# Kernel optimization log

Measured on AMD Instinct MI355X. Metric: run time of the kernel, lower is better.

## Reference

```python
import jax, jax.numpy as jnp
import numpy as np

H = 512      # hidden_size
Z = 128      # z_dim
E = 512      # embedding_dim
D = 2 * H + Z  # GRU hidden / decoder state dim = 1152
V = 32000    # output_size
BS = 256
N = 128      # encoder nodes per source


def setup_inputs() -> dict:
    key = jax.random.key(0)
    ks = jax.random.split(key, 24)
    s = 0.05
    inp = {
        "prev_y": jax.random.normal(ks[0], (BS, E), jnp.float32),
        "prev_h": jax.random.normal(ks[1], (BS, D), jnp.float32),
        "equ_enc": jax.random.normal(ks[2], (BS, N, H), jnp.float32),
        "sns_enc": jax.random.normal(ks[3], (BS, N, H), jnp.float32),
        "z_sample": jax.random.normal(ks[4], (BS, Z), jnp.float32),
        "equ_mask": jax.random.randint(ks[5], (BS, N), 0, 2) > 0,
        "sns_mask": jax.random.randint(ks[6], (BS, N), 0, 2) > 0,
        # Attention (equ): W1: HxH, W2: HxD, vt: 1xH (torch Linear weight = [out,in])
        "W1e": jax.random.normal(ks[7], (H, H), jnp.float32) * s,
        "W2e": jax.random.normal(ks[8], (H, D), jnp.float32) * s,
        "vte": jax.random.normal(ks[9], (1, H), jnp.float32) * s,
        "W1s": jax.random.normal(ks[10], (H, H), jnp.float32) * s,
        "W2s": jax.random.normal(ks[11], (H, D), jnp.float32) * s,
        "vts": jax.random.normal(ks[12], (1, H), jnp.float32) * s,
        "plan_W": jax.random.normal(ks[13], (2, D), jnp.float32) * s,
        "plan_b": jax.random.normal(ks[14], (2,), jnp.float32) * s,
        "Wc": jax.random.normal(ks[15], (H, E + H), jnp.float32) * s,
        "bc": jax.random.normal(ks[16], (H,), jnp.float32) * s,
        # GRU: input H -> hidden D
        "w_ih": jax.random.normal(ks[17], (3 * D, H), jnp.float32) * s,
        "w_hh": jax.random.normal(ks[18], (3 * D, D), jnp.float32) * s,
        "b_ih": jax.random.normal(ks[19], (3 * D,), jnp.float32) * s,
        "b_hh": jax.random.normal(ks[20], (3 * D,), jnp.float32) * s,
        "Wout": jax.random.normal(ks[21], (V, D), jnp.float32) * s,
        "bout": jax.random.normal(ks[22], (V,), jnp.float32) * s,
    }
    return inp


def _attn(h, enc, mask, W1, W2, vt):
    # enc: (b,n,H), h: (b,D)
    et = jnp.einsum('bnh,kh->bnk', enc, W1)          # (b,n,H)
    dt = (h @ W2.T)[:, None, :]                       # (b,1,H)
    u = jnp.einsum('bnh,h->bn', jnp.tanh(et + dt), vt[0])
    u = jnp.where(mask, -jnp.inf, u)
    return jax.nn.softmax(u, axis=-1)                 # (b,n)


def reference(prev_y, prev_h, equ_enc, sns_enc, z_sample, equ_mask, sns_mask,
              W1e, W2e, vte, W1s, W2s, vts, plan_W, plan_b, Wc, bc,
              w_ih, w_hh, b_ih, b_hh, Wout, bout):
    aw_e = _attn(prev_h, equ_enc, equ_mask, W1e, W2e, vte)
    ctx_e = jnp.einsum('bn,bnh->bh', aw_e, equ_enc)
    aw_s = _attn(prev_h, sns_enc, sns_mask, W1s, W2s, vts)
    ctx_s = jnp.einsum('bn,bnh->bh', aw_s, sns_enc)
    plan = jax.nn.softmax(prev_h @ plan_W.T + plan_b, axis=-1)  # (b,2)
    combine = jnp.stack([ctx_e, ctx_s], axis=1)                  # (b,2,H)
    context = jnp.einsum('bk,bkh->bh', plan, combine)
    y_ctx = jnp.concatenate([prev_y, context], axis=-1)          # (b,E+H)
    x = y_ctx @ Wc.T + bc                                        # (b,H)
    # single-step GRU (torch gate order: r, z, n)
    gx = x @ w_ih.T + b_ih                                       # (b,3D)
    gh = prev_h @ w_hh.T + b_hh
    Dh = prev_h.shape[-1]
    gx_r, gx_z, gx_n = gx[:, :Dh], gx[:, Dh:2*Dh], gx[:, 2*Dh:]
    gh_r, gh_z, gh_n = gh[:, :Dh], gh[:, Dh:2*Dh], gh[:, 2*Dh:]
    r = jax.nn.sigmoid(gx_r + gh_r)
    zg = jax.nn.sigmoid(gx_z + gh_z)
    n = jnp.tanh(gx_n + r * gh_n)
    h_new = (1.0 - zg) * n + zg * prev_h                          # (b,D)
    dec_output = (h_new @ Wout.T + bout)[:, None, :]              # (b,1,V)
    dec_hidden = h_new[None]                                      # (1,b,D)
    return dec_output, dec_hidden, plan
```

## Files before the change

kernel.cpp:

```cpp
#include <hip/hip_runtime.h>
#include <stdint.h>
#include <math.h>

#define BS_  256
#define NSEQ 128
#define HH   512
#define DD   1152
#define VV   32000
#define BN_  (BS_*NSEQ)

typedef float  f32x4  __attribute__((ext_vector_type(4)));
typedef __bf16 bf16x8 __attribute__((ext_vector_type(8)));

__device__ __forceinline__ f32x4 mfma16(bf16x8 a, bf16x8 b, f32x4 c) {
    return __builtin_amdgcn_mfma_f32_16x16x32_bf16(a, b, c, 0, 0, 0);
}

__device__ __forceinline__ bf16x8 pack8(f32x4 a, f32x4 b) {
    bf16x8 v;
    v[0] = (__bf16)a[0]; v[1] = (__bf16)a[1]; v[2] = (__bf16)a[2]; v[3] = (__bf16)a[3];
    v[4] = (__bf16)b[0]; v[5] = (__bf16)b[1]; v[6] = (__bf16)b[2]; v[7] = (__bf16)b[3];
    return v;
}

__global__ __launch_bounds__(256) void k_gemm_bias(
    const float* __restrict__ A, const float* __restrict__ B,
    const float* __restrict__ bias, float* __restrict__ C,
    int K, int ldc)
{
    const int cb = blockIdx.x * 64;
    const int rb = blockIdx.y * 64;
    const int t  = threadIdx.x;
    const int w = t >> 6, lane = t & 63, g = lane >> 4, r = lane & 15;
    const int s_row = t >> 2, s_kc = t & 3;

    __shared__ bf16x8 sm[2][2][256];

    const float* Ap = A + (size_t)(rb + s_row) * K + s_kc * 8;
    const float* Bp = B + (size_t)(cb + s_row) * K + s_kc * 8;

    const int KS = K >> 5;
    f32x4 pa0 = *(const f32x4*)Ap, pa1 = *(const f32x4*)(Ap + 4);
    f32x4 pb0 = *(const f32x4*)Bp, pb1 = *(const f32x4*)(Bp + 4);

    f32x4 acc[4] = {{0,0,0,0},{0,0,0,0},{0,0,0,0},{0,0,0,0}};

    for (int kb = 0; kb < KS; ++kb) {
        sm[kb & 1][0][s_kc * 64 + s_row] = pack8(pa0, pa1);
        sm[kb & 1][1][s_kc * 64 + s_row] = pack8(pb0, pb1);
        __syncthreads();
        if (kb + 1 < KS) {
            const float* a2 = Ap + (kb + 1) * 32;
            const float* b2 = Bp + (kb + 1) * 32;
            pa0 = *(const f32x4*)a2; pa1 = *(const f32x4*)(a2 + 4);
            pb0 = *(const f32x4*)b2; pb1 = *(const f32x4*)(b2 + 4);
        }
        bf16x8 af = sm[kb & 1][0][g * 64 + w * 16 + r];
        #pragma unroll
        for (int j = 0; j < 4; ++j) {
            bf16x8 bf = sm[kb & 1][1][g * 64 + j * 16 + r];
            acc[j] = mfma16(af, bf, acc[j]);
        }
    }
    #pragma unroll
    for (int j = 0; j < 4; ++j) {
        int col = cb + j * 16 + r;
        float bv = bias ? bias[col] : 0.f;
        #pragma unroll
        for (int q = 0; q < 4; ++q) {
            int row = rb + w * 16 + g * 4 + q;
            C[(size_t)row * ldc + col] = acc[j][q] + bv;
        }
    }
}

__global__ __launch_bounds__(256) void k_prevh(
    const float* __restrict__ prev_h, const float* __restrict__ W2e,
    const float* __restrict__ W2s, const float* __restrict__ w_hh,
    const float* __restrict__ b_hh,
    float* __restrict__ dt_e, float* __restrict__ dt_s, float* __restrict__ gh)
{
    const int cb = blockIdx.x * 64;
    const int rb = blockIdx.y * 64;
    const int t  = threadIdx.x;
    const int w = t >> 6, lane = t & 63, g = lane >> 4, r = lane & 15;
    const int s_row = t >> 2, s_kc = t & 3;
    const int K = DD;

    __shared__ bf16x8 sm[2][2][256];

    const float* Ap = prev_h + (size_t)(rb + s_row) * K + s_kc * 8;
    const float* Bp;
    {
        int brow = cb + s_row;
        if (cb < 512)        Bp = W2e + (size_t)brow * K;
        else if (cb < 1024)  Bp = W2s + (size_t)(brow - 512) * K;
        else                 Bp = w_hh + (size_t)(brow - 1024) * K;
        Bp += s_kc * 8;
    }

    const int KS = K >> 5;
    f32x4 pa0 = *(const f32x4*)Ap, pa1 = *(const f32x4*)(Ap + 4);
    f32x4 pb0 = *(const f32x4*)Bp, pb1 = *(const f32x4*)(Bp + 4);

    f32x4 acc[4] = {{0,0,0,0},{0,0,0,0},{0,0,0,0},{0,0,0,0}};

    for (int kb = 0; kb < KS; ++kb) {
        sm[kb & 1][0][s_kc * 64 + s_row] = pack8(pa0, pa1);
        sm[kb & 1][1][s_kc * 64 + s_row] = pack8(pb0, pb1);
        __syncthreads();
        if (kb + 1 < KS) {
            const float* a2 = Ap + (kb + 1) * 32;
            const float* b2 = Bp + (kb + 1) * 32;
            pa0 = *(const f32x4*)a2; pa1 = *(const f32x4*)(a2 + 4);
            pb0 = *(const f32x4*)b2; pb1 = *(const f32x4*)(b2 + 4);
        }
        bf16x8 af = sm[kb & 1][0][g * 64 + w * 16 + r];
        #pragma unroll
        for (int j = 0; j < 4; ++j) {
            bf16x8 bf = sm[kb & 1][1][g * 64 + j * 16 + r];
            acc[j] = mfma16(af, bf, acc[j]);
        }
    }

    #pragma unroll
    for (int j = 0; j < 4; ++j) {
        int col = cb + j * 16 + r;
        #pragma unroll
        for (int q = 0; q < 4; ++q) {
            int row = rb + w * 16 + g * 4 + q;
            float v = acc[j][q];
            if (cb < 512)       dt_e[(size_t)row * 512 + col] = v;
            else if (cb < 1024) dt_s[(size_t)row * 512 + (col - 512)] = v;
            else {
                int c0 = col - 1024;
                gh[(size_t)row * 3456 + c0] = v + b_hh[c0];
            }
        }
    }
}

__global__ __launch_bounds__(512) void k_attn_u(
    const float* __restrict__ enc_e, const float* __restrict__ enc_s,
    const float* __restrict__ W1e, const float* __restrict__ W1s,
    const float* __restrict__ vte, const float* __restrict__ vts,
    const float* __restrict__ dt_e, const float* __restrict__ dt_s,
    float* __restrict__ u)
{
    extern __shared__ char smem_raw[];
    bf16x8* As  = (bf16x8*)smem_raw;
    bf16x8* Bs  = (bf16x8*)(smem_raw + 65536);
    float*  dts = (float*)(smem_raw + 131072);
    float*  vtl = dts + 512;
    float*  uacc = vtl + 512;

    const int e = blockIdx.y;
    const float* enc = e ? enc_s : enc_e;
    const float* W1  = e ? W1s : W1e;
    const float* vt  = e ? vts : vte;
    const float* dt  = e ? dt_s : dt_e;

    const int rowbase = blockIdx.x * 64;
    const int b = rowbase >> 7;
    const int t = threadIdx.x;
    const int w = t >> 6, lane = t & 63, g = lane >> 4, r = lane & 15;

    if (t < 64) uacc[t] = 0.f;
    dts[t] = dt[(size_t)b * 512 + t];
    vtl[t] = vt[t];

    #pragma unroll
    for (int i = 0; i < 8; ++i) {
        int row = w * 8 + i;
        const float* src = enc + (size_t)(rowbase + row) * 512 + lane * 8;
        f32x4 x0 = *(const f32x4*)src;
        f32x4 x1 = *(const f32x4*)(src + 4);
        As[lane * 64 + (row ^ (lane & 15))] = pack8(x0, x1);
    }

    f32x4 p0[4], p1[4];
    {
        int cc = 0, kb = 0;
        #pragma unroll
        for (int jj = 0; jj < 4; ++jj) {
            int c = t + 512 * jj;
            int col = c >> 3, kc = c & 7;
            const float* src = W1 + (size_t)(cc * 256 + col) * 512 + kb * 64 + kc * 8;
            p0[jj] = *(const f32x4*)src;
            p1[jj] = *(const f32x4*)(src + 4);
        }
    }

    f32x4 acc[4][2];
    #pragma unroll
    for (int i = 0; i < 4; ++i) { acc[i][0] = (f32x4){0,0,0,0}; acc[i][1] = (f32x4){0,0,0,0}; }

    for (int s = 0; s < 16; ++s) {
        bf16x8* Bb = Bs + (s & 1) * 2048;
        #pragma unroll
        for (int jj = 0; jj < 4; ++jj) {
            int c = t + 512 * jj;
            int col = c >> 3, kc = c & 7;
            Bb[kc * 256 + col] = pack8(p0[jj], p1[jj]);
        }
        __syncthreads();
        if (s + 1 < 16) {
            int cc2 = (s + 1) >> 3, kb2 = (s + 1) & 7;
            #pragma unroll
            for (int jj = 0; jj < 4; ++jj) {
                int c = t + 512 * jj;
                int col = c >> 3, kc = c & 7;
                const float* src = W1 + (size_t)(cc2 * 256 + col) * 512 + kb2 * 64 + kc * 8;
                p0[jj] = *(const f32x4*)src;
                p1[jj] = *(const f32x4*)(src + 4);
            }
        }
        int kb = s & 7;
        #pragma unroll
        for (int kk = 0; kk < 2; ++kk) {
            int kg = kb * 8 + kk * 4 + g;
            bf16x8 bf0 = Bb[(kk * 4 + g) * 256 + w * 32 + r];
            bf16x8 bf1 = Bb[(kk * 4 + g) * 256 + w * 32 + 16 + r];
            #pragma unroll
            for (int i = 0; i < 4; ++i) {
                bf16x8 af = As[kg * 64 + (16 * i + (r ^ (kg & 15)))];
                acc[i][0] = mfma16(af, bf0, acc[i][0]);
                acc[i][1] = mfma16(af, bf1, acc[i][1]);
            }
        }
        if ((s & 7) == 7) {
            int cc = s >> 3;
            #pragma unroll
            for (int i = 0; i < 4; ++i) {
                float ps0 = 0.f, ps1 = 0.f, ps2 = 0.f, ps3 = 0.f;
                #pragma unroll
                for (int j = 0; j < 2; ++j) {
                    int col = cc * 256 + w * 32 + j * 16 + r;
                    float dv = dts[col], vv = vtl[col];
                    ps0 += vv * tanhf(acc[i][j][0] + dv);
                    ps1 += vv * tanhf(acc[i][j][1] + dv);
                    ps2 += vv * tanhf(acc[i][j][2] + dv);
                    ps3 += vv * tanhf(acc[i][j][3] + dv);
                }
                #pragma unroll
                for (int m = 1; m < 16; m <<= 1) {
                    ps0 += __shfl_xor(ps0, m);
                    ps1 += __shfl_xor(ps1, m);
                    ps2 += __shfl_xor(ps2, m);
                    ps3 += __shfl_xor(ps3, m);
                }
                if (r == 0) {
                    atomicAdd(&uacc[16 * i + 4 * g + 0], ps0);
                    atomicAdd(&uacc[16 * i + 4 * g + 1], ps1);
                    atomicAdd(&uacc[16 * i + 4 * g + 2], ps2);
                    atomicAdd(&uacc[16 * i + 4 * g + 3], ps3);
                }
                acc[i][0] = (f32x4){0,0,0,0};
                acc[i][1] = (f32x4){0,0,0,0};
            }
        }
    }
    __syncthreads();
    if (t < 64) u[(size_t)e * BN_ + rowbase + t] = uacc[t];
}

__global__ __launch_bounds__(256) void k_ctx(
    const float* __restrict__ u, const int* __restrict__ mask_e,
    const int* __restrict__ mask_s, const float* __restrict__ enc_e,
    const float* __restrict__ enc_s, const float* __restrict__ prev_h,
    const float* __restrict__ plan_W, const float* __restrict__ plan_b,
    const float* __restrict__ prev_y,
    float* __restrict__ y_ctx, float* __restrict__ plan_out)
{
    const int b = blockIdx.x;
    const int t = threadIdx.x;
    const int lane = t & 63, wid = t >> 6, half = t >> 7, n = t & 127;

    __shared__ float aw[2][128];
    __shared__ float red[16];
    __shared__ float planv[2];

    const int* mask = half ? mask_s : mask_e;
    float uv = u[(size_t)half * BN_ + b * 128 + n];
    bool msk = mask[b * 128 + n] != 0;
    float val = msk ? -3.4e38f : uv;

    float mx = val;
    #pragma unroll
    for (int m = 1; m < 64; m <<= 1) mx = fmaxf(mx, __shfl_xor(mx, m));
    if (lane == 0) red[wid] = mx;
    __syncthreads();
    mx = fmaxf(red[half * 2], red[half * 2 + 1]);
    float ex = msk ? 0.f : __expf(uv - mx);
    float sm = ex;
    #pragma unroll
    for (int m = 1; m < 64; m <<= 1) sm += __shfl_xor(sm, m);
    if (lane == 0) red[4 + wid] = sm;
    __syncthreads();
    sm = red[4 + half * 2] + red[4 + half * 2 + 1];
    aw[half][n] = ex / sm;

    float p0 = 0.f, p1 = 0.f;
    for (int i = t; i < DD; i += 256) {
        float hv = prev_h[(size_t)b * DD + i];
        p0 += hv * plan_W[i];
        p1 += hv * plan_W[DD + i];
    }
    #pragma unroll
    for (int m = 1; m < 64; m <<= 1) { p0 += __shfl_xor(p0, m); p1 += __shfl_xor(p1, m); }
    if (lane == 0) { red[8 + wid] = p0; red[12 + wid] = p1; }
    __syncthreads();
    if (t == 0) {
        float l0 = red[8] + red[9] + red[10] + red[11] + plan_b[0];
        float l1 = red[12] + red[13] + red[14] + red[15] + plan_b[1];
        float mm = fmaxf(l0, l1);
        float e0 = __expf(l0 - mm), e1 = __expf(l1 - mm);
        float ss = e0 + e1;
        planv[0] = e0 / ss; planv[1] = e1 / ss;
        plan_out[b * 2 + 0] = planv[0];
        plan_out[b * 2 + 1] = planv[1];
    }
    __syncthreads();

    float pl0 = planv[0], pl1 = planv[1];
    #pragma unroll
    for (int cc = 0; cc < 2; ++cc) {
        int col = t + cc * 256;
        float ae = 0.f, as2 = 0.f;
        const float* pe = enc_e + (size_t)b * 128 * 512 + col;
        const float* ps = enc_s + (size_t)b * 128 * 512 + col;
        #pragma unroll 4
        for (int nn = 0; nn < 128; ++nn) {
            ae  += aw[0][nn] * pe[(size_t)nn * 512];
            as2 += aw[1][nn] * ps[(size_t)nn * 512];
        }
        float ctx = pl0 * ae + pl1 * as2;
        y_ctx[(size_t)b * 1024 + col] = prev_y[(size_t)b * 512 + col];
        y_ctx[(size_t)b * 1024 + 512 + col] = ctx;
    }
}

__global__ __launch_bounds__(384) void k_gru(
    const float* __restrict__ gx, const float* __restrict__ gh,
    const float* __restrict__ prev_h, float* __restrict__ h_new,
    float* __restrict__ out_hidden)
{
    int d = blockIdx.x * 384 + threadIdx.x;
    int b = blockIdx.y;
    size_t o3 = (size_t)b * 3456;
    float xr = gx[o3 + d], xz = gx[o3 + 1152 + d], xn = gx[o3 + 2304 + d];
    float hr = gh[o3 + d], hz = gh[o3 + 1152 + d], hn = gh[o3 + 2304 + d];
    float rr = 1.f / (1.f + __expf(-(xr + hr)));
    float zz = 1.f / (1.f + __expf(-(xz + hz)));
    float nv = tanhf(xn + rr * hn);
    float hv = (1.f - zz) * nv + zz * prev_h[(size_t)b * DD + d];
    h_new[(size_t)b * DD + d] = hv;
    out_hidden[(size_t)b * DD + d] = hv;
}

extern "C" void kernel_launch(void* const* d_in, const int* in_sizes, int n_in,
                              void* d_out, int out_size, void* d_ws, size_t ws_size,
                              hipStream_t stream)
{
    const float* prev_y = (const float*)d_in[0];
    const float* prev_h = (const float*)d_in[1];
    const float* enc_e  = (const float*)d_in[2];
    const float* enc_s  = (const float*)d_in[3];
    const int*   mask_e = (const int*)d_in[5];
    const int*   mask_s = (const int*)d_in[6];
    const float* W1e    = (const float*)d_in[7];
    const float* W2e    = (const float*)d_in[8];
    const float* vte    = (const float*)d_in[9];
    const float* W1s    = (const float*)d_in[10];
    const float* W2s    = (const float*)d_in[11];
    const float* vts    = (const float*)d_in[12];
    const float* plan_W = (const float*)d_in[13];
    const float* plan_b = (const float*)d_in[14];
    const float* Wc     = (const float*)d_in[15];
    const float* bc     = (const float*)d_in[16];
    const float* w_ih   = (const float*)d_in[17];
    const float* w_hh   = (const float*)d_in[18];
    const float* b_ih   = (const float*)d_in[19];
    const float* b_hh   = (const float*)d_in[20];
    const float* Wout   = (const float*)d_in[21];
    const float* bout   = (const float*)d_in[22];

    float* out = (float*)d_out;
    float* ws  = (float*)d_ws;
    float* dt_e  = ws;
    float* dt_s  = dt_e + 131072;
    float* gh    = dt_s + 131072;
    float* uu    = gh + 884736;
    float* y_ctx = uu + 65536;
    float* xx    = y_ctx + 262144;
    float* gx    = xx + 131072;
    float* h_new = gx + 884736;

    float* dec_out  = out;
    float* dec_hid  = out + 8192000;
    float* plan_out = out + 8486912;

    k_prevh<<<dim3(70, 4), 256, 0, stream>>>(prev_h, W2e, W2s, w_hh, b_hh,
                                             dt_e, dt_s, gh);

    (void)hipFuncSetAttribute((const void*)k_attn_u,
                              hipFuncAttributeMaxDynamicSharedMemorySize, 143360);
    k_attn_u<<<dim3(BN_ / 64, 2), 512, 135424, stream>>>(
        enc_e, enc_s, W1e, W1s, vte, vts, dt_e, dt_s, uu);

    k_ctx<<<dim3(BS_), 256, 0, stream>>>(uu, mask_e, mask_s, enc_e, enc_s,
                                         prev_h, plan_W, plan_b, prev_y,
                                         y_ctx, plan_out);

    k_gemm_bias<<<dim3(8, 4), 256, 0, stream>>>(y_ctx, Wc, bc, xx, 1024, 512);
    k_gemm_bias<<<dim3(54, 4), 256, 0, stream>>>(xx, w_ih, b_ih, gx, 512, 3456);

    k_gru<<<dim3(3, BS_), 384, 0, stream>>>(gx, gh, prev_h, h_new, dec_hid);

    k_gemm_bias<<<dim3(500, 4), 256, 0, stream>>>(h_new, Wout, bout, dec_out,
                                                  1152, 32000);
}
```

Baseline: 641.8 us.

## Use 128x128 MFMA tiles for large GEMMs and restructure attention and context kernels

Measured after the change: 575.0 us. -10.4%, faster.

```diff
diff --git a/kernel.cpp b/kernel.cpp
--- a/kernel.cpp
+++ b/kernel.cpp
@@ -23,21 +23,117 @@
     return v;
 }
 
-__global__ __launch_bounds__(256) void k_gemm_bias(
+__device__ __forceinline__ float tanh_fast(float x) {
+    float e = __expf(2.f * x);
+    return 1.f - __fdividef(2.f, e + 1.f);
+}
+
+__global__ __launch_bounds__(256) void k_tile128(
     const float* __restrict__ A, const float* __restrict__ B,
     const float* __restrict__ bias, float* __restrict__ C,
     int K, int ldc)
+{
+    const int rb = blockIdx.x * 128;
+    const int cb = blockIdx.y * 128;
+    const int t = threadIdx.x;
+    const int w = t >> 6, wr = w >> 1, wc = w & 1;
+    const int lane = t & 63, g = lane >> 4, r = lane & 15;
+    const int s_row = t >> 1, s_h = t & 1;
+
+    __shared__ bf16x8 sm[2][2][512];
+
+    const float* Ap = A + (size_t)(rb + s_row) * K + s_h * 16;
+    const float* Bp = B + (size_t)(cb + s_row) * K + s_h * 16;
+
+    const int kg0 = 2 * s_h, kg1 = 2 * s_h + 1;
+    const int swz0 = kg0 * 128 + ((s_row & 112) | ((s_row ^ (kg0 << 2)) & 15));
+    const int swz1 = kg1 * 128 + ((s_row & 112) | ((s_row ^ (kg1 << 2)) & 15));
+
+    int ai[4], bi[4];
+    #pragma unroll
+    for (int i = 0; i < 4; ++i) {
+        ai[i] = g * 128 + wr * 64 + i * 16 + ((r ^ (g << 2)) & 15);
+        bi[i] = g * 128 + wc * 64 + i * 16 + ((r ^ (g << 2)) & 15);
+    }
+
+    const int KS = K >> 5;
+    f32x4 pa0 = ((const f32x4*)Ap)[0], pa1 = ((const f32x4*)Ap)[1],
+          pa2 = ((const f32x4*)Ap)[2], pa3 = ((const f32x4*)Ap)[3];
+    f32x4 pb0 = ((const f32x4*)Bp)[0], pb1 = ((const f32x4*)Bp)[1],
+          pb2 = ((const f32x4*)Bp)[2], pb3 = ((const f32x4*)Bp)[3];
+
+    f32x4 acc[4][4];
+    #pragma unroll
+    for (int i = 0; i < 4; ++i)
+        #pragma unroll
+        for (int j = 0; j < 4; ++j) acc[i][j] = (f32x4){0.f, 0.f, 0.f, 0.f};
+
+    for (int kb = 0; kb < KS; ++kb) {
+        const int buf = kb & 1;
+        sm[buf][0][swz0] = pack8(pa0, pa1);
+        sm[buf][0][swz1] = pack8(pa2, pa3);
+        sm[buf][1][swz0] = pack8(pb0, pb1);
+        sm[buf][1][swz1] = pack8(pb2, pb3);
+        __syncthreads();
+        if (kb + 1 < KS) {
+            const float* a2 = Ap + (kb + 1) * 32;
+            const float* b2 = Bp + (kb + 1) * 32;
+            pa0 = ((const f32x4*)a2)[0]; pa1 = ((const f32x4*)a2)[1];
+            pa2 = ((const f32x4*)a2)[2]; pa3 = ((const f32x4*)a2)[3];
+            pb0 = ((const f32x4*)b2)[0]; pb1 = ((const f32x4*)b2)[1];
+            pb2 = ((const f32x4*)b2)[2]; pb3 = ((const f32x4*)b2)[3];
+        }
+        bf16x8 af[4], bfr[4];
+        #pragma unroll
+        for (int i = 0; i < 4; ++i) af[i]  = sm[buf][0][ai[i]];
+        #pragma unroll
+        for (int j = 0; j < 4; ++j) bfr[j] = sm[buf][1][bi[j]];
+        #pragma unroll
+        for (int i = 0; i < 4; ++i)
+            #pragma unroll
+            for (int j = 0; j < 4; ++j)
+                acc[i][j] = mfma16(af[i], bfr[j], acc[i][j]);
+    }
+
+    #pragma unroll
+    for (int j = 0; j < 4; ++j) {
+        const int col = cb + wc * 64 + j * 16 + r;
+        const float bv = bias ? bias[col] : 0.f;
+        #pragma unroll
+        for (int i = 0; i < 4; ++i) {
+            #pragma unroll
+            for (int q = 0; q < 4; ++q) {
+                const int row = rb + wr * 64 + i * 16 + g * 4 + q;
+                C[(size_t)row * ldc + col] = acc[i][j][q] + bv;
+            }
+        }
+    }
+}
+
+__global__ __launch_bounds__(256) void k_prevh(
+    const float* __restrict__ prev_h, const float* __restrict__ W2e,
+    const float* __restrict__ W2s, const float* __restrict__ w_hh,
+    const float* __restrict__ b_hh,
+    float* __restrict__ dt_e, float* __restrict__ dt_s, float* __restrict__ gh)
 {
     const int cb = blockIdx.x * 64;
     const int rb = blockIdx.y * 64;
     const int t  = threadIdx.x;
     const int w = t >> 6, lane = t & 63, g = lane >> 4, r = lane & 15;
     const int s_row = t >> 2, s_kc = t & 3;
+    const int K = DD;
 
     __shared__ bf16x8 sm[2][2][256];
 
-    const float* Ap = A + (size_t)(rb + s_row) * K + s_kc * 8;
-    const float* Bp = B + (size_t)(cb + s_row) * K + s_kc * 8;
+    const float* Ap = prev_h + (size_t)(rb + s_row) * K + s_kc * 8;
+    const float* Bp;
+    {
+        int brow = cb + s_row;
+        if (cb < 512)        Bp = W2e + (size_t)brow * K;
+        else if (cb < 1024)  Bp = W2s + (size_t)(brow - 512) * K;
+        else                 Bp = w_hh + (size_t)(brow - 1024) * K;
+        Bp += s_kc * 8;
+    }
 
     const int KS = K >> 5;
     f32x4 pa0 = *(const f32x4*)Ap, pa1 = *(const f32x4*)(Ap + 4);
@@ -62,66 +158,6 @@
             acc[j] = mfma16(af, bf, acc[j]);
         }
     }
-    #pragma unroll
-    for (int j = 0; j < 4; ++j) {
-        int col = cb + j * 16 + r;
-        float bv = bias ? bias[col] : 0.f;
-        #pragma unroll
-        for (int q = 0; q < 4; ++q) {
-            int row = rb + w * 16 + g * 4 + q;
-            C[(size_t)row * ldc + col] = acc[j][q] + bv;
-        }
-    }
-}
-
-__global__ __launch_bounds__(256) void k_prevh(
-    const float* __restrict__ prev_h, const float* __restrict__ W2e,
-    const float* __restrict__ W2s, const float* __restrict__ w_hh,
-    const float* __restrict__ b_hh,
-    float* __restrict__ dt_e, float* __restrict__ dt_s, float* __restrict__ gh)
-{
-    const int cb = blockIdx.x * 64;
-    const int rb = blockIdx.y * 64;
-    const int t  = threadIdx.x;
-    const int w = t >> 6, lane = t & 63, g = lane >> 4, r = lane & 15;
-    const int s_row = t >> 2, s_kc = t & 3;
-    const int K = DD;
-
-    __shared__ bf16x8 sm[2][2][256];
-
-    const float* Ap = prev_h + (size_t)(rb + s_row) * K + s_kc * 8;
-    const float* Bp;
-    {
-        int brow = cb + s_row;
-        if (cb < 512)        Bp = W2e + (size_t)brow * K;
-        else if (cb < 1024)  Bp = W2s + (size_t)(brow - 512) * K;
-        else                 Bp = w_hh + (size_t)(brow - 1024) * K;
-        Bp += s_kc * 8;
-    }
-
-    const int KS = K >> 5;
-    f32x4 pa0 = *(const f32x4*)Ap, pa1 = *(const f32x4*)(Ap + 4);
-    f32x4 pb0 = *(const f32x4*)Bp, pb1 = *(const f32x4*)(Bp + 4);
-
-    f32x4 acc[4] = {{0,0,0,0},{0,0,0,0},{0,0,0,0},{0,0,0,0}};
-
-    for (int kb = 0; kb < KS; ++kb) {
-        sm[kb & 1][0][s_kc * 64 + s_row] = pack8(pa0, pa1);
-        sm[kb & 1][1][s_kc * 64 + s_row] = pack8(pb0, pb1);
-        __syncthreads();
-        if (kb + 1 < KS) {
-            const float* a2 = Ap + (kb + 1) * 32;
-            const float* b2 = Bp + (kb + 1) * 32;
-            pa0 = *(const f32x4*)a2; pa1 = *(const f32x4*)(a2 + 4);
-            pb0 = *(const f32x4*)b2; pb1 = *(const f32x4*)(b2 + 4);
-        }
-        bf16x8 af = sm[kb & 1][0][g * 64 + w * 16 + r];
-        #pragma unroll
-        for (int j = 0; j < 4; ++j) {
-            bf16x8 bf = sm[kb & 1][1][g * 64 + j * 16 + r];
-            acc[j] = mfma16(af, bf, acc[j]);
-        }
-    }
 
     #pragma unroll
     for (int j = 0; j < 4; ++j) {
@@ -140,128 +176,114 @@
     }
 }
 
-__global__ __launch_bounds__(512) void k_attn_u(
+__global__ __launch_bounds__(256) void k_attn(
     const float* __restrict__ enc_e, const float* __restrict__ enc_s,
     const float* __restrict__ W1e, const float* __restrict__ W1s,
     const float* __restrict__ vte, const float* __restrict__ vts,
     const float* __restrict__ dt_e, const float* __restrict__ dt_s,
     float* __restrict__ u)
 {
-    extern __shared__ char smem_raw[];
-    bf16x8* As  = (bf16x8*)smem_raw;
-    bf16x8* Bs  = (bf16x8*)(smem_raw + 65536);
-    float*  dts = (float*)(smem_raw + 131072);
-    float*  vtl = dts + 512;
-    float*  uacc = vtl + 512;
-
+    const int b = blockIdx.x;
     const int e = blockIdx.y;
     const float* enc = e ? enc_s : enc_e;
-    const float* W1  = e ? W1s : W1e;
-    const float* vt  = e ? vts : vte;
+    const float* W1  = e ? W1s  : W1e;
+    const float* vt  = e ? vts  : vte;
     const float* dt  = e ? dt_s : dt_e;
 
-    const int rowbase = blockIdx.x * 64;
-    const int b = rowbase >> 7;
+    __shared__ bf16x8 sm[2][2][512];
+    __shared__ float uacc[128];
+
     const int t = threadIdx.x;
-    const int w = t >> 6, lane = t & 63, g = lane >> 4, r = lane & 15;
-
-    if (t < 64) uacc[t] = 0.f;
-    dts[t] = dt[(size_t)b * 512 + t];
-    vtl[t] = vt[t];
-
-    #pragma unroll
-    for (int i = 0; i < 8; ++i) {
-        int row = w * 8 + i;
-        const float* src = enc + (size_t)(rowbase + row) * 512 + lane * 8;
-        f32x4 x0 = *(const f32x4*)src;
-        f32x4 x1 = *(const f32x4*)(src + 4);
-        As[lane * 64 + (row ^ (lane & 15))] = pack8(x0, x1);
-    }
-
-    f32x4 p0[4], p1[4];
+    const int w = t >> 6, wr = w >> 1, wc = w & 1;
+    const int lane = t & 63, g = lane >> 4, r = lane & 15;
+    const int s_row = t >> 1, s_h = t & 1;
+
+    if (t < 128) uacc[t] = 0.f;
+
+    const int kg0 = 2 * s_h, kg1 = 2 * s_h + 1;
+    const int swz0 = kg0 * 128 + ((s_row & 112) | ((s_row ^ (kg0 << 2)) & 15));
+    const int swz1 = kg1 * 128 + ((s_row & 112) | ((s_row ^ (kg1 << 2)) & 15));
+
+    int ai[4], bi[4];
+    #pragma unroll
+    for (int i = 0; i < 4; ++i) {
+        ai[i] = g * 128 + wr * 64 + i * 16 + ((r ^ (g << 2)) & 15);
+        bi[i] = g * 128 + wc * 64 + i * 16 + ((r ^ (g << 2)) & 15);
+    }
+
+    const float* Abase = enc + (size_t)(b * 128 + s_row) * 512 + s_h * 16;
+
+    f32x4 pa0, pa1, pa2, pa3, pb0, pb1, pb2, pb3;
     {
-        int cc = 0, kb = 0;
-        #pragma unroll
-        for (int jj = 0; jj < 4; ++jj) {
-            int c = t + 512 * jj;
-            int col = c >> 3, kc = c & 7;
-            const float* src = W1 + (size_t)(cc * 256 + col) * 512 + kb * 64 + kc * 8;
-            p0[jj] = *(const f32x4*)src;
-            p1[jj] = *(const f32x4*)(src + 4);
-        }
-    }
-
-    f32x4 acc[4][2];
-    #pragma unroll
-    for (int i = 0; i < 4; ++i) { acc[i][0] = (f32x4){0,0,0,0}; acc[i][1] = (f32x4){0,0,0,0}; }
-
-    for (int s = 0; s < 16; ++s) {
-        bf16x8* Bb = Bs + (s & 1) * 2048;
-        #pragma unroll
-        for (int jj = 0; jj < 4; ++jj) {
-            int c = t + 512 * jj;
-            int col = c >> 3, kc = c & 7;
-            Bb[kc * 256 + col] = pack8(p0[jj], p1[jj]);
-        }
-        __syncthreads();
-        if (s + 1 < 16) {
-            int cc2 = (s + 1) >> 3, kb2 = (s + 1) & 7;
-            #pragma unroll
-            for (int jj = 0; jj < 4; ++jj) {
-                int c = t + 512 * jj;
-                int col = c >> 3, kc = c & 7;
-                const float* src = W1 + (size_t)(cc2 * 256 + col) * 512 + kb2 * 64 + kc * 8;
-                p0[jj] = *(const f32x4*)src;
-                p1[jj] = *(const f32x4*)(src + 4);
+        const float* ap = Abase;
+        const float* bp = W1 + (size_t)s_row * 512 + s_h * 16;
+        pa0 = ((const f32x4*)ap)[0]; pa1 = ((const f32x4*)ap)[1];
+        pa2 = ((const f32x4*)ap)[2]; pa3 = ((const f32x4*)ap)[3];
+        pb0 = ((const f32x4*)bp)[0]; pb1 = ((const f32x4*)bp)[1];
+        pb2 = ((const f32x4*)bp)[2]; pb3 = ((const f32x4*)bp)[3];
+    }
+
+    for (int nc = 0; nc < 4; ++nc) {
+        f32x4 acc[4][4];
+        #pragma unroll
+        for (int i = 0; i < 4; ++i)
+            #pragma unroll
+            for (int j = 0; j < 4; ++j) acc[i][j] = (f32x4){0.f, 0.f, 0.f, 0.f};
+
+        for (int kb = 0; kb < 16; ++kb) {
+            const int buf = kb & 1;
+            sm[buf][0][swz0] = pack8(pa0, pa1);
+            sm[buf][0][swz1] = pack8(pa2, pa3);
+            sm[buf][1][swz0] = pack8(pb0, pb1);
+            sm[buf][1][swz1] = pack8(pb2, pb3);
+            __syncthreads();
+
+            int nnc = nc, nkb = kb + 1;
+            if (nkb == 16) { nnc = nc + 1; nkb = 0; }
+            if (nnc < 4) {
+                const float* ap = Abase + nkb * 32;
+                const float* bp = W1 + (size_t)(nnc * 128 + s_row) * 512 + nkb * 32 + s_h * 16;
+                pa0 = ((const f32x4*)ap)[0]; pa1 = ((const f32x4*)ap)[1];
+                pa2 = ((const f32x4*)ap)[2]; pa3 = ((const f32x4*)ap)[3];
+                pb0 = ((const f32x4*)bp)[0]; pb1 = ((const f32x4*)bp)[1];
+                pb2 = ((const f32x4*)bp)[2]; pb3 = ((const f32x4*)bp)[3];
             }
-        }
-        int kb = s & 7;
-        #pragma unroll
-        for (int kk = 0; kk < 2; ++kk) {
-            int kg = kb * 8 + kk * 4 + g;
-            bf16x8 bf0 = Bb[(kk * 4 + g) * 256 + w * 32 + r];
-            bf16x8 bf1 = Bb[(kk * 4 + g) * 256 + w * 32 + 16 + r];
-            #pragma unroll
-            for (int i = 0; i < 4; ++i) {
-                bf16x8 af = As[kg * 64 + (16 * i + (r ^ (kg & 15)))];
-                acc[i][0] = mfma16(af, bf0, acc[i][0]);
-                acc[i][1] = mfma16(af, bf1, acc[i][1]);
+
+            bf16x8 af[4], bfr[4];
+            #pragma unroll
+            for (int i = 0; i < 4; ++i) af[i]  = sm[buf][0][ai[i]];
+            #pragma unroll
+            for (int j = 0; j < 4; ++j) bfr[j] = sm[buf][1][bi[j]];
+            #pragma unroll
+            for (int i = 0; i < 4; ++i)
+                #pragma unroll
+                for (int j = 0; j < 4; ++j)
+                    acc[i][j] = mfma16(af[i], bfr[j], acc[i][j]);
+        }
+
+        float dv[4], vv[4];
+        #pragma unroll
+        for (int j = 0; j < 4; ++j) {
+            int col = nc * 128 + wc * 64 + j * 16 + r;
+            dv[j] = dt[(size_t)b * 512 + col];
+            vv[j] = vt[col];
+        }
+        #pragma unroll
+        for (int i = 0; i < 4; ++i) {
+            #pragma unroll
+            for (int q = 0; q < 4; ++q) {
+                float s = 0.f;
+                #pragma unroll
+                for (int j = 0; j < 4; ++j)
+                    s += vv[j] * tanh_fast(acc[i][j][q] + dv[j]);
+                #pragma unroll
+                for (int m = 1; m < 16; m <<= 1) s += __shfl_xor(s, m);
+                if (r == 0) atomicAdd(&uacc[wr * 64 + i * 16 + g * 4 + q], s);
             }
         }
-        if ((s & 7) == 7) {
-            int cc = s >> 3;
-            #pragma unroll
-            for (int i = 0; i < 4; ++i) {
-                float ps0 = 0.f, ps1 = 0.f, ps2 = 0.f, ps3 = 0.f;
-                #pragma unroll
-                for (int j = 0; j < 2; ++j) {
-                    int col = cc * 256 + w * 32 + j * 16 + r;
-                    float dv = dts[col], vv = vtl[col];
-                    ps0 += vv * tanhf(acc[i][j][0] + dv);
-                    ps1 += vv * tanhf(acc[i][j][1] + dv);
-                    ps2 += vv * tanhf(acc[i][j][2] + dv);
-                    ps3 += vv * tanhf(acc[i][j][3] + dv);
-                }
-                #pragma unroll
-                for (int m = 1; m < 16; m <<= 1) {
-                    ps0 += __shfl_xor(ps0, m);
-                    ps1 += __shfl_xor(ps1, m);
-                    ps2 += __shfl_xor(ps2, m);
-                    ps3 += __shfl_xor(ps3, m);
-                }
-                if (r == 0) {
-                    atomicAdd(&uacc[16 * i + 4 * g + 0], ps0);
-                    atomicAdd(&uacc[16 * i + 4 * g + 1], ps1);
-                    atomicAdd(&uacc[16 * i + 4 * g + 2], ps2);
-                    atomicAdd(&uacc[16 * i + 4 * g + 3], ps3);
-                }
-                acc[i][0] = (f32x4){0,0,0,0};
-                acc[i][1] = (f32x4){0,0,0,0};
-            }
-        }
     }
     __syncthreads();
-    if (t < 64) u[(size_t)e * BN_ + rowbase + t] = uacc[t];
+    if (t < 128) u[(size_t)e * BN_ + b * 128 + t] = uacc[t];
 }
 
 __global__ __launch_bounds__(256) void k_ctx(
@@ -323,20 +345,68 @@
     __syncthreads();
 
     float pl0 = planv[0], pl1 = planv[1];
-    #pragma unroll
-    for (int cc = 0; cc < 2; ++cc) {
-        int col = t + cc * 256;
-        float ae = 0.f, as2 = 0.f;
-        const float* pe = enc_e + (size_t)b * 128 * 512 + col;
-        const float* ps = enc_s + (size_t)b * 128 * 512 + col;
-        #pragma unroll 4
-        for (int nn = 0; nn < 128; ++nn) {
-            ae  += aw[0][nn] * pe[(size_t)nn * 512];
-            as2 += aw[1][nn] * ps[(size_t)nn * 512];
-        }
-        float ctx = pl0 * ae + pl1 * as2;
-        y_ctx[(size_t)b * 1024 + col] = prev_y[(size_t)b * 512 + col];
-        y_ctx[(size_t)b * 1024 + 512 + col] = ctx;
+    int col = blockIdx.y * 256 + t;
+    float ae = 0.f, as2 = 0.f;
+    const float* pe = enc_e + (size_t)b * 128 * 512 + col;
+    const float* ps = enc_s + (size_t)b * 128 * 512 + col;
+    #pragma unroll 8
+    for (int nn = 0; nn < 128; ++nn) {
+        ae  += aw[0][nn] * pe[(size_t)nn * 512];
+        as2 += aw[1][nn] * ps[(size_t)nn * 512];
+    }
+    float ctx = pl0 * ae + pl1 * as2;
+    y_ctx[(size_t)b * 1024 + col] = prev_y[(size_t)b * 512 + col];
+    y_ctx[(size_t)b * 1024 + 512 + col] = ctx;
+}
+
+__global__ __launch_bounds__(256) void k_gemm_bias(
+    const float* __restrict__ A, const float* __restrict__ B,
+    const float* __restrict__ bias, float* __restrict__ C,
+    int K, int ldc)
+{
+    const int cb = blockIdx.x * 64;
+    const int rb = blockIdx.y * 64;
+    const int t  = threadIdx.x;
+    const int w = t >> 6, lane = t & 63, g = lane >> 4, r = lane & 15;
+    const int s_row = t >> 2, s_kc = t & 3;
+
+    __shared__ bf16x8 sm[2][2][256];
+
+    const float* Ap = A + (size_t)(rb + s_row) * K + s_kc * 8;
+    const float* Bp = B + (size_t)(cb + s_row) * K + s_kc * 8;
+
+    const int KS = K >> 5;
+    f32x4 pa0 = *(const f32x4*)Ap, pa1 = *(const f32x4*)(Ap + 4);
+    f32x4 pb0 = *(const f32x4*)Bp, pb1 = *(const f32x4*)(Bp + 4);
+
+    f32x4 acc[4] = {{0,0,0,0},{0,0,0,0},{0,0,0,0},{0,0,0,0}};
+
+    for (int kb = 0; kb < KS; ++kb) {
+        sm[kb & 1][0][s_kc * 64 + s_row] = pack8(pa0, pa1);
+        sm[kb & 1][1][s_kc * 64 + s_row] = pack8(pb0, pb1);
+        __syncthreads();
+        if (kb + 1 < KS) {
+            const float* a2 = Ap + (kb + 1) * 32;
+            const float* b2 = Bp + (kb + 1) * 32;
+            pa0 = *(const f32x4*)a2; pa1 = *(const f32x4*)(a2 + 4);
+            pb0 = *(const f32x4*)b2; pb1 = *(const f32x4*)(b2 + 4);
+        }
+        bf16x8 af = sm[kb & 1][0][g * 64 + w * 16 + r];
+        #pragma unroll
+        for (int j = 0; j < 4; ++j) {
+            bf16x8 bf = sm[kb & 1][1][g * 64 + j * 16 + r];
+            acc[j] = mfma16(af, bf, acc[j]);
+        }
+    }
+    #pragma unroll
+    for (int j = 0; j < 4; ++j) {
+        int col = cb + j * 16 + r;
+        float bv = bias ? bias[col] : 0.f;
+        #pragma unroll
+        for (int q = 0; q < 4; ++q) {
+            int row = rb + w * 16 + g * 4 + q;
+            C[(size_t)row * ldc + col] = acc[j][q] + bv;
+        }
     }
 }
 
@@ -403,20 +473,18 @@
     k_prevh<<<dim3(70, 4), 256, 0, stream>>>(prev_h, W2e, W2s, w_hh, b_hh,
                                              dt_e, dt_s, gh);
 
-    (void)hipFuncSetAttribute((const void*)k_attn_u,
-                              hipFuncAttributeMaxDynamicSharedMemorySize, 143360);
-    k_attn_u<<<dim3(BN_ / 64, 2), 512, 135424, stream>>>(
+    k_attn<<<dim3(BS_, 2), 256, 0, stream>>>(
         enc_e, enc_s, W1e, W1s, vte, vts, dt_e, dt_s, uu);
 
-    k_ctx<<<dim3(BS_), 256, 0, stream>>>(uu, mask_e, mask_s, enc_e, enc_s,
-                                         prev_h, plan_W, plan_b, prev_y,
-                                         y_ctx, plan_out);
+    k_ctx<<<dim3(BS_, 2), 256, 0, stream>>>(uu, mask_e, mask_s, enc_e, enc_s,
+                                            prev_h, plan_W, plan_b, prev_y,
+                                            y_ctx, plan_out);
 
     k_gemm_bias<<<dim3(8, 4), 256, 0, stream>>>(y_ctx, Wc, bc, xx, 1024, 512);
-    k_gemm_bias<<<dim3(54, 4), 256, 0, stream>>>(xx, w_ih, b_ih, gx, 512, 3456);
+    k_tile128<<<dim3(2, 27), 256, 0, stream>>>(xx, w_ih, b_ih, gx, 512, 3456);
 
     k_gru<<<dim3(3, BS_), 384, 0, stream>>>(gx, gh, prev_h, h_new, dec_hid);
 
-    k_gemm_bias<<<dim3(500, 4), 256, 0, stream>>>(h_new, Wout, bout, dec_out,
-                                                  1152, 32000);
-}
+    k_tile128<<<dim3(2, 250), 256, 0, stream>>>(h_new, Wout, bout, dec_out,
+                                                1152, 32000);
+}
```
